# Kernel optimization log

Measured on AMD Instinct MI355X. Metric: run time of the kernel, lower is better.

## Reference

```python
import jax, jax.numpy as jnp
import numpy as np

NUM_TOKENS = 32
PAD_TOKEN = 1
DEL_COST = 1.0
INF = 1e9
EPS = 1e-7


def setup_inputs() -> dict:
    key = jax.random.key(0)
    k1, k2 = jax.random.split(key)
    y_true = jax.random.randint(k1, (32, 512), 0, NUM_TOKENS)
    y_pred = jax.random.uniform(k2, (32, 1024, NUM_TOKENS), dtype=jnp.float32)
    return {"y_true": y_true, "y_pred": y_pred}


def _left_shift(seq, pad_token):
    # remove internal pad tokens, shift real tokens left (stable)
    L = seq.shape[1]
    ixs = jnp.arange(L)
    keys = jnp.where(seq != pad_token, ixs[None, :], L + ixs[None, :])
    order = jnp.sort(keys, axis=1) % L
    return jnp.take_along_axis(seq, order, axis=1)


def _alignment(subs, ins, seq_lens):
    # subs: [b, m, n] substitution costs; ins: [b, n] insertion costs
    b, m, n = subs.shape
    dt = subs.dtype

    # wavefrontify subs -> [m+n-1, m, b]: out[k, i, :] = subs[:, i, k-i] (0 if oob)
    ks = jnp.arange(m + n - 1)[:, None]
    ii = jnp.arange(m)[None, :]
    jj = ks - ii
    subs_t = jnp.transpose(subs, (1, 2, 0))  # [m, n, b]
    subs_wf = jnp.where((jj >= 0) & (jj < n)[..., None] if False else ((jj >= 0) & (jj < n))[..., None],
                        subs_t[ii, jnp.clip(jj, 0, n - 1)], jnp.zeros((), dt))

    # wavefrontify ins -> [m+n, m+1, b]: out[k, i, :] = ins[:, k-i] (0 if oob)
    ks2 = jnp.arange(m + n)[:, None]
    ii2 = jnp.arange(m + 1)[None, :]
    jj2 = ks2 - ii2
    ins_t = jnp.transpose(ins, (1, 0))  # [n, b]
    ins_wf = jnp.where(((jj2 >= 0) & (jj2 < n))[..., None],
                       ins_t[jnp.clip(jj2, 0, n - 1)], jnp.zeros((), dt))

    i_range = jnp.arange(m + 1)
    batch_idx = jnp.arange(b)
    k_end = seq_lens + n  # antidiagonal where each sequence's answer lives

    # k=0 wavefront: D[0][0]=0 ; k=1 wavefront: D[0][1]=ins[0], D[1][0]=del
    v_p2 = jnp.concatenate([jnp.zeros((1, b), dt), jnp.full((m - 1, b), INF, dt)], 0)
    v_p1 = jnp.concatenate([ins_wf[0][:1], jnp.full((1, b), DEL_COST, dt),
                            jnp.full((m - 1, b), INF, dt)], 0)
    v_opt = jnp.full((b,), INF, dt)

    def step(carry, xs):
        v_p2, v_p1, v_opt = carry
        k, sub_k, ins_k = xs
        o_m = v_p2 + sub_k            # match:  D[i][j] + subs -> row i+1
        o_i = v_p1 + ins_k            # insert: D[i][j-1] + ins[j-1]
        v_p2n = v_p1[:-1]
        o_d = v_p2n + DEL_COST        # delete: D[i-1][j] + del
        rest = jnp.minimum(jnp.minimum(o_m, o_i[1:]), o_d)
        v_p1n = jnp.concatenate([o_i[:1], rest], 0)
        mask = ((k - i_range) >= 0) & ((k - i_range) <= n)
        v_p1n = jnp.where(mask[:, None], v_p1n, jnp.full((), INF, dt))
        v_opt = jnp.where(k_end == k, v_p1n[seq_lens, batch_idx], v_opt)
        return (v_p2n, v_p1n, v_opt), None

    ks_seq = jnp.arange(2, m + n + 1)
    (_, _, v_opt), _ = jax.lax.scan(step, (v_p2, v_p1, v_opt),
                                    (ks_seq, subs_wf, ins_wf[1:]))
    return v_opt


def reference(y_true, y_pred):
    y_true_ls = _left_shift(y_true, PAD_TOKEN)
    seq_lens = jnp.sum((y_true_ls != PAD_TOKEN).astype(jnp.int32), axis=-1)
    y_oh = jax.nn.one_hot(y_true_ls, NUM_TOKENS, dtype=y_pred.dtype)
    y_p = y_pred / jnp.sum(y_pred, axis=-1, keepdims=True)
    logp = jnp.log(jnp.clip(y_p, EPS, 1.0 - EPS))  # [b, n, t]
    subs = -jnp.einsum('bmt,bnt->bmn', y_oh, logp)  # sparse xent cost matrix
    ins = -jnp.log(jnp.clip(y_p[..., PAD_TOKEN], EPS, 1.0 - EPS))  # [b, n]
    loss = _alignment(subs, ins, seq_lens)
    return loss.sum()  # reduction='sum'
```

## Files before the change

### kernel.cpp

```cpp
#include <hip/hip_runtime.h>

#define NTOK 32
#define PADT 1
#define MLEN 512
#define NLEN 1024
#define EPS_F 1e-7f
#define CCH 256
#define NC 4
#define NWAVE 4
#define BSTRIDE 416

#define OFF_BND   0
#define OFF_P0    (OFF_BND + 4*2*BSTRIDE)
#define OFF_TOK   (OFF_P0 + 1184)
#define OFF_WTMP  (OFF_TOK + 512)
#define OFF_NL    (OFF_WTMP + 16)
#define LDS_FLOATS (OFF_NL + NTOK*NLEN + 160)

template <bool MASKED>
__device__ __forceinline__ void do_iter2(
    const float2*& q0, const float2*& q1, const float2*& qi, const float2*& qb,
    float2 (&C0)[8], float2 (&C1)[8], float2 (&CI)[8], float2 (&CB)[8],
    float2 (&N0)[8], float2 (&N1)[8], float2 (&NI)[8], float2 (&NB)[8],
    float& s0, float& s1, float& pA, float& dgA,
    int& sb, const int lane, float2* __restrict__ bw2)
{
#pragma unroll
  for (int k = 0; k < 8; ++k) {
    N0[k] = q0[8 + k]; N1[k] = q1[8 + k];
    NI[k] = qi[8 + k]; NB[k] = qb[8 + k];
  }
#pragma unroll
  for (int k = 0; k < 8; ++k) {
    float upA = __int_as_float(__builtin_amdgcn_update_dpp(
        __float_as_int(CB[k].x), __float_as_int(pA), 0x138, 0xF, 0xF, false));
    float upB = __int_as_float(__builtin_amdgcn_update_dpp(
        __float_as_int(CB[k].y), __float_as_int(s1), 0x138, 0xF, 0xF, false));
    float mA0 = fminf(fminf(dgA + C0[k].x, upA + 1.0f), s0 + CI[k].x);
    float mB0 = fminf(fminf(upA + C0[k].y, upB + 1.0f), mA0 + CI[k].y);
    float mA1 = fminf(fminf(s0  + C1[k].x, mA0 + 1.0f), s1 + CI[k].x);
    float mB1 = fminf(fminf(mA0 + C1[k].y, mB0 + 1.0f), mA1 + CI[k].y);
    if (lane == 63) {
      int sl = sb + k - 63;
      if (MASKED) sl = sl < 0 ? 0 : sl;
      bw2[sl] = make_float2(mA1, mB1);
    }
    if (MASKED) {
      int rsk = sb + k - lane;
      bool act = ((unsigned)rsk) < 128u;
      dgA = (rsk < 128) ? upB : dgA;
      s0 = act ? mB0 : s0;
      pA = act ? mA1 : pA;
      s1 = act ? mB1 : s1;
    } else {
      dgA = upB; s0 = mB0; pA = mA1; s1 = mB1;
    }
  }
  q0 += 8; q1 += 8; qi += 8; qb += 8; sb += 8;
}

__global__ __launch_bounds__(256, 1) void align_loss_kernel(
    const int* __restrict__ y_true, const float* __restrict__ y_pred,
    float* __restrict__ partial)
{
  extern __shared__ float smem[];
  float* bnd   = smem + OFF_BND;
  float* P0arr = smem + OFF_P0;
  int*   tok   = (int*)(smem + OFF_TOK);
  float* wtmp  = smem + OFF_WTMP;
  int*   wti   = (int*)wtmp;
  float* nl    = smem + OFF_NL;

  const int b = blockIdx.x;
  const int t = threadIdx.x;
  const int lane = t & 63;
  const int wv = t >> 6;

  tok[t] = 0; tok[t + 256] = 0;
  __syncthreads();
  int total = 0;
  for (int h = 0; h < 2; ++h) {
    int yt = y_true[b * MLEN + h * 256 + t];
    bool f = (yt != PADT);
    unsigned long long m = __ballot(f);
    int wp = __popcll(m & ((1ull << lane) - 1ull));
    if (lane == 0) wti[8 + wv] = __popcll(m);
    __syncthreads();
    int offs = total, ht = 0;
#pragma unroll
    for (int w2 = 0; w2 < NWAVE; ++w2) { int cnt = wti[8 + w2]; if (w2 < wv) offs += cnt; ht += cnt; }
    if (f) tok[offs + wp] = yt;
    total += ht;
    __syncthreads();
  }
  const int L = total;

  for (int r = t; r < NLEN; r += 256) {
    const float4* rp = (const float4*)(y_pred + ((size_t)b * NLEN + r) * NTOK);
    float4 q[8]; float s = 0.f;
#pragma unroll
    for (int u = 0; u < 8; ++u) { q[u] = rp[u]; s += q[u].x + q[u].y + q[u].z + q[u].w; }
    float inv = 1.0f / s;
#pragma unroll
    for (int u = 0; u < 8; ++u) {
      float pv[4] = {q[u].x, q[u].y, q[u].z, q[u].w};
#pragma unroll
      for (int c2 = 0; c2 < 4; ++c2) {
        float p = pv[c2] * inv;
        p = fminf(fmaxf(p, EPS_F), 1.0f - EPS_F);
        nl[(u * 4 + c2) * NLEN + r] = -__logf(p);
      }
    }
  }
  __syncthreads();

  {
    float4 iv = *(const float4*)(nl + PADT * NLEN + 4 * t);
    float p1 = iv.x, p2 = iv.x + iv.y, p3 = p2 + iv.z, s4 = p3 + iv.w;
    float x = s4;
#pragma unroll
    for (int d = 1; d < 64; d <<= 1) {
      float y = __shfl_up(x, d);
      if (lane >= d) x += y;
    }
    if (lane == 63) wtmp[wv] = x;
    __syncthreads();
    float pre = x - s4;
#pragma unroll
    for (int w2 = 0; w2 < NWAVE; ++w2) if (w2 < wv) pre += wtmp[w2];
    *(float4*)(P0arr + 4 * t) = make_float4(pre + p1, pre + p2, pre + p3, pre + s4);
  }

  const int r0 = 2 * t + 1;
  const int tk0 = tok[2 * t];
  const int tk1 = tok[2 * t + 1];
  const float* sub0 = nl + tk0 * NLEN;
  const float* sub1 = nl + tk1 * NLEN;
  const float* insp = nl + PADT * NLEN;
  float s0  = (float)r0;
  float s1  = (float)(r0 + 1);
  float dgA = (float)(r0 - 1);
  float pA  = (float)(r0 + 1);

  for (int p = 0; p < NC + NWAVE - 1; ++p) {
    __syncthreads();
    const int c = p - wv;
    if (c < 0 || c >= NC) continue;
    const int base = c * CCH;
    const float2* q0 = (const float2*)(sub0 + base) - lane;
    const float2* q1 = (const float2*)(sub1 + base) - lane;
    const float2* qi = (const float2*)(insp + base) - lane;
    const float2* qb = (wv == 0) ? (const float2*)(P0arr + base)
                                 : (const float2*)(bnd + ((wv - 1) * 2 + (p & 1)) * BSTRIDE);
    float2* bw2 = (float2*)(bnd + (wv * 2 + ((p + 1) & 1)) * BSTRIDE);

    float2 A0[8], A1[8], AI[8], AB[8], B0[8], B1[8], BI[8], BB[8];
#pragma unroll
    for (int k = 0; k < 8; ++k) { A0[k] = q0[k]; A1[k] = q1[k]; AI[k] = qi[k]; AB[k] = qb[k]; }
    int sb = 0;
    for (int it2 = 0; it2 < 4; ++it2) {
      do_iter2<true>(q0, q1, qi, qb, A0, A1, AI, AB, B0, B1, BI, BB, s0, s1, pA, dgA, sb, lane, bw2);
      do_iter2<true>(q0, q1, qi, qb, B0, B1, BI, BB, A0, A1, AI, AB, s0, s1, pA, dgA, sb, lane, bw2);
    }
    for (int it2 = 0; it2 < 4; ++it2) {
      do_iter2<false>(q0, q1, qi, qb, A0, A1, AI, AB, B0, B1, BI, BB, s0, s1, pA, dgA, sb, lane, bw2);
      do_iter2<false>(q0, q1, qi, qb, B0, B1, BI, BB, A0, A1, AI, AB, s0, s1, pA, dgA, sb, lane, bw2);
    }
    for (int it2 = 0; it2 < 4; ++it2) {
      do_iter2<true>(q0, q1, qi, qb, A0, A1, AI, AB, B0, B1, BI, BB, s0, s1, pA, dgA, sb, lane, bw2);
      do_iter2<true>(q0, q1, qi, qb, B0, B1, BI, BB, A0, A1, AI, AB, s0, s1, pA, dgA, sb, lane, bw2);
    }
  }

  if (r0 == L) partial[b] = s0;
  if (r0 + 1 == L) partial[b] = s1;
  if (L == 0 && t == 0) partial[b] = P0arr[NLEN - 1];
}

__global__ void reduce_kernel(const float* __restrict__ partial, float* __restrict__ out) {
  if (threadIdx.x == 0) {
    float s = 0.f;
    for (int b2 = 0; b2 < 32; ++b2) s += partial[b2];
    out[0] = s;
  }
}

extern "C" void kernel_launch(void* const* d_in, const int* in_sizes, int n_in,
                              void* d_out, int out_size, void* d_ws, size_t ws_size,
                              hipStream_t stream) {
  const int*   y_true = (const int*)d_in[0];
  const float* y_pred = (const float*)d_in[1];
  float* out = (float*)d_out;
  float* partial = (float*)d_ws;

  const size_t lds_bytes = (size_t)LDS_FLOATS * sizeof(float);
  hipFuncSetAttribute((const void*)align_loss_kernel,
                      hipFuncAttributeMaxDynamicSharedMemorySize, (int)lds_bytes);

  hipLaunchKernelGGL(align_loss_kernel, dim3(32), dim3(256), lds_bytes, stream,
                     y_true, y_pred, partial);
  hipLaunchKernelGGL(reduce_kernel, dim3(1), dim3(64), 0, stream, partial, out);
}
```

Measured before the change: 101.8 us.

## Transpose DP parallelization: lanes own prediction columns, sweep token rows

The wavefront DP is reorganized so that each lane owns four consecutive prediction positions (columns) and iterates over token rows in chunks of 128. Previously each lane owned two token rows and swept the prediction axis. Substitution costs are now fetched as float4 from the per-token log-prob table indexed by the row token, and the insertion cost becomes a per-lane constant. Boundary values pass between waves through LDS as float4 column-edge writes, and the answer is captured when the row index equals the sequence length. The aim is more work per lane per DPP shift and fewer LDS reads, at the price of token-indexed gathers and a new boundary protocol.

```diff
diff --git a/kernel.cpp b/kernel.cpp
--- a/kernel.cpp
+++ b/kernel.cpp
@@ -5,58 +5,79 @@
 #define MLEN 512
 #define NLEN 1024
 #define EPS_F 1e-7f
-#define CCH 256
-#define NC 4
+
+#define RCH 128
+#define NC  4
 #define NWAVE 4
-#define BSTRIDE 416
-
-#define OFF_BND   0
-#define OFF_P0    (OFF_BND + 4*2*BSTRIDE)
-#define OFF_TOK   (OFF_P0 + 1184)
-#define OFF_WTMP  (OFF_TOK + 512)
-#define OFF_NL    (OFF_WTMP + 16)
-#define LDS_FLOATS (OFF_NL + NTOK*NLEN + 160)
+#define NPHASE (NC + NWAVE - 1)
+
+#define OFF_P0   0
+#define OFF_BND  1024
+#define OFF_BNDZ (OFF_BND + 6*256)
+#define OFF_TOK  (OFF_BNDZ + 256)
+#define OFF_WT   (OFF_TOK + 736)
+#define OFF_NL   (OFF_WT + 16)
+#define LDS_FLOATS (OFF_NL + NTOK*NLEN)
+
+__device__ __forceinline__ float min3f(float a, float b, float c) {
+  return fminf(fminf(a, b), c);
+}
+__device__ __forceinline__ float dpp_shr1(float old_v, float src) {
+  return __int_as_float(__builtin_amdgcn_update_dpp(
+      __float_as_int(old_v), __float_as_int(src), 0x138, 0xF, 0xF, false));
+}
 
 template <bool MASKED>
-__device__ __forceinline__ void do_iter2(
-    const float2*& q0, const float2*& q1, const float2*& qi, const float2*& qb,
-    float2 (&C0)[8], float2 (&C1)[8], float2 (&CI)[8], float2 (&CB)[8],
-    float2 (&N0)[8], float2 (&N1)[8], float2 (&NI)[8], float2 (&NB)[8],
-    float& s0, float& s1, float& pA, float& dgA,
-    int& sb, const int lane, float2* __restrict__ bw2)
+__device__ __forceinline__ void do_iter(
+    int s0, int lane, int wv,
+    const int* __restrict__ tokl, const float* __restrict__ nlJ,
+    const float* __restrict__ bndR, float* __restrict__ bndW,
+    int (&TKc)[8], float4 (&SBc)[8], int (&TKn)[8], float4 (&SBn)[8],
+    float4 ri,
+    float& vp0, float& vp1, float& vp2, float& vp3,
+    float& dgL, float& m3p,
+    float& wq0, float& wq1, float& wq2, float& wq3,
+    float& ans, int qh)
 {
 #pragma unroll
+  for (int k = 0; k < 8; ++k) TKn[k] = tokl[s0 + 16 + k];
+#pragma unroll
+  for (int k = 0; k < 8; ++k)
+    SBn[k] = *(const float4*)(nlJ + ((size_t)((unsigned)TKc[k]) << 10));
+  float4 ja = *(const float4*)(bndR + s0);
+  float4 jb = *(const float4*)(bndR + s0 + 4);
+  float inj[8] = {ja.x, ja.y, ja.z, ja.w, jb.x, jb.y, jb.z, jb.w};
+  const int q0 = s0 - lane;
+#pragma unroll
   for (int k = 0; k < 8; ++k) {
-    N0[k] = q0[8 + k]; N1[k] = q1[8 + k];
-    NI[k] = qi[8 + k]; NB[k] = qb[8 + k];
-  }
-#pragma unroll
-  for (int k = 0; k < 8; ++k) {
-    float upA = __int_as_float(__builtin_amdgcn_update_dpp(
-        __float_as_int(CB[k].x), __float_as_int(pA), 0x138, 0xF, 0xF, false));
-    float upB = __int_as_float(__builtin_amdgcn_update_dpp(
-        __float_as_int(CB[k].y), __float_as_int(s1), 0x138, 0xF, 0xF, false));
-    float mA0 = fminf(fminf(dgA + C0[k].x, upA + 1.0f), s0 + CI[k].x);
-    float mB0 = fminf(fminf(upA + C0[k].y, upB + 1.0f), mA0 + CI[k].y);
-    float mA1 = fminf(fminf(s0  + C1[k].x, mA0 + 1.0f), s1 + CI[k].x);
-    float mB1 = fminf(fminf(mA0 + C1[k].y, mB0 + 1.0f), mA1 + CI[k].y);
-    if (lane == 63) {
-      int sl = sb + k - 63;
-      if (MASKED) sl = sl < 0 ? 0 : sl;
-      bw2[sl] = make_float2(mA1, mB1);
-    }
+    const int q = q0 + k;
+    float Lnow = dpp_shr1(inj[k], m3p);
+    float m0 = min3f(dgL + SBc[k].x, vp0 + 1.0f, Lnow + ri.x);
+    float m1 = min3f(vp0 + SBc[k].y, vp1 + 1.0f, m0 + ri.y);
+    float m2 = min3f(vp1 + SBc[k].z, vp2 + 1.0f, m1 + ri.z);
+    float m3 = min3f(vp2 + SBc[k].w, vp3 + 1.0f, m2 + ri.w);
     if (MASKED) {
-      int rsk = sb + k - lane;
-      bool act = ((unsigned)rsk) < 128u;
-      dgA = (rsk < 128) ? upB : dgA;
-      s0 = act ? mB0 : s0;
-      pA = act ? mA1 : pA;
-      s1 = act ? mB1 : s1;
+      bool act = ((unsigned)q) < 128u;
+      bool lt  = (q < 128);
+      dgL = lt ? Lnow : dgL;
+      vp0 = act ? m0 : vp0;  vp1 = act ? m1 : vp1;
+      vp2 = act ? m2 : vp2;  vp3 = act ? m3 : vp3;
+      m3p = act ? m3 : m3p;
+      if (act && q == qh) ans = m3;
     } else {
-      dgA = upB; s0 = mB0; pA = mA1; s1 = mB1;
-    }
-  }
-  q0 += 8; q1 += 8; qi += 8; qb += 8; sb += 8;
+      dgL = Lnow; vp0 = m0; vp1 = m1; vp2 = m2; vp3 = m3; m3p = m3;
+      if (q == qh) ans = m3;
+    }
+    switch ((k + 1) & 3) {
+      case 0: wq0 = m3; break; case 1: wq1 = m3; break;
+      case 2: wq2 = m3; break; case 3: wq3 = m3; break;
+    }
+    if (k == 2 || k == 6) {
+      int q63 = s0 + k - 63;
+      if (wv < 3 && lane == 63 && q63 >= 3 && q63 < 128)
+        *(float4*)(bndW + (q63 - 3)) = make_float4(wq0, wq1, wq2, wq3);
+    }
+  }
 }
 
 __global__ __launch_bounds__(256, 1) void align_loss_kernel(
@@ -64,10 +85,12 @@
     float* __restrict__ partial)
 {
   extern __shared__ float smem[];
+  float* P0    = smem + OFF_P0;
   float* bnd   = smem + OFF_BND;
-  float* P0arr = smem + OFF_P0;
-  int*   tok   = (int*)(smem + OFF_TOK);
-  float* wtmp  = smem + OFF_WTMP;
+  float* bndZ  = smem + OFF_BNDZ;
+  int*   tokbuf= (int*)(smem + OFF_TOK);
+  int*   tokg  = tokbuf + 64;
+  float* wtmp  = smem + OFF_WT;
   int*   wti   = (int*)wtmp;
   float* nl    = smem + OFF_NL;
 
@@ -76,8 +99,9 @@
   const int lane = t & 63;
   const int wv = t >> 6;
 
-  tok[t] = 0; tok[t + 256] = 0;
+  for (int idx = t; idx < 736; idx += 256) tokbuf[idx] = 0;
   __syncthreads();
+
   int total = 0;
   for (int h = 0; h < 2; ++h) {
     int yt = y_true[b * MLEN + h * 256 + t];
@@ -89,7 +113,7 @@
     int offs = total, ht = 0;
 #pragma unroll
     for (int w2 = 0; w2 < NWAVE; ++w2) { int cnt = wti[8 + w2]; if (w2 < wv) offs += cnt; ht += cnt; }
-    if (f) tok[offs + wp] = yt;
+    if (f) tokg[offs + wp] = yt;
     total += ht;
     __syncthreads();
   }
@@ -128,53 +152,66 @@
     float pre = x - s4;
 #pragma unroll
     for (int w2 = 0; w2 < NWAVE; ++w2) if (w2 < wv) pre += wtmp[w2];
-    *(float4*)(P0arr + 4 * t) = make_float4(pre + p1, pre + p2, pre + p3, pre + s4);
-  }
-
-  const int r0 = 2 * t + 1;
-  const int tk0 = tok[2 * t];
-  const int tk1 = tok[2 * t + 1];
-  const float* sub0 = nl + tk0 * NLEN;
-  const float* sub1 = nl + tk1 * NLEN;
-  const float* insp = nl + PADT * NLEN;
-  float s0  = (float)r0;
-  float s1  = (float)(r0 + 1);
-  float dgA = (float)(r0 - 1);
-  float pA  = (float)(r0 + 1);
-
-  for (int p = 0; p < NC + NWAVE - 1; ++p) {
+    *(float4*)(P0 + 4 * t) = make_float4(pre + p1, pre + p2, pre + p3, pre + s4);
+  }
+  __syncthreads();
+
+  const int J = 256 * wv + 4 * lane;
+  const float* nlJ = nl + J;
+  float4 ri = *(const float4*)(nl + PADT * NLEN + J);
+  float4 vpi = *(const float4*)(P0 + J);
+  float vp0 = vpi.x, vp1 = vpi.y, vp2 = vpi.z, vp3 = vpi.w;
+  float m3p = vp3;
+  float dgL = 0.0f;
+  if (J > 0) dgL = P0[J - 1];
+  float wq0 = 0, wq1 = 0, wq2 = 0, wq3 = 0, ans = 0.0f;
+
+  for (int p = 0; p < NPHASE; ++p) {
     __syncthreads();
     const int c = p - wv;
     if (c < 0 || c >= NC) continue;
-    const int base = c * CCH;
-    const float2* q0 = (const float2*)(sub0 + base) - lane;
-    const float2* q1 = (const float2*)(sub1 + base) - lane;
-    const float2* qi = (const float2*)(insp + base) - lane;
-    const float2* qb = (wv == 0) ? (const float2*)(P0arr + base)
-                                 : (const float2*)(bnd + ((wv - 1) * 2 + (p & 1)) * BSTRIDE);
-    float2* bw2 = (float2*)(bnd + (wv * 2 + ((p + 1) & 1)) * BSTRIDE);
-
-    float2 A0[8], A1[8], AI[8], AB[8], B0[8], B1[8], BI[8], BB[8];
-#pragma unroll
-    for (int k = 0; k < 8; ++k) { A0[k] = q0[k]; A1[k] = q1[k]; AI[k] = qi[k]; AB[k] = qb[k]; }
-    int sb = 0;
-    for (int it2 = 0; it2 < 4; ++it2) {
-      do_iter2<true>(q0, q1, qi, qb, A0, A1, AI, AB, B0, B1, BI, BB, s0, s1, pA, dgA, sb, lane, bw2);
-      do_iter2<true>(q0, q1, qi, qb, B0, B1, BI, BB, A0, A1, AI, AB, s0, s1, pA, dgA, sb, lane, bw2);
-    }
-    for (int it2 = 0; it2 < 4; ++it2) {
-      do_iter2<false>(q0, q1, qi, qb, A0, A1, AI, AB, B0, B1, BI, BB, s0, s1, pA, dgA, sb, lane, bw2);
-      do_iter2<false>(q0, q1, qi, qb, B0, B1, BI, BB, A0, A1, AI, AB, s0, s1, pA, dgA, sb, lane, bw2);
-    }
-    for (int it2 = 0; it2 < 4; ++it2) {
-      do_iter2<true>(q0, q1, qi, qb, A0, A1, AI, AB, B0, B1, BI, BB, s0, s1, pA, dgA, sb, lane, bw2);
-      do_iter2<true>(q0, q1, qi, qb, B0, B1, BI, BB, A0, A1, AI, AB, s0, s1, pA, dgA, sb, lane, bw2);
-    }
-  }
-
-  if (r0 == L) partial[b] = s0;
-  if (r0 + 1 == L) partial[b] = s1;
-  if (L == 0 && t == 0) partial[b] = P0arr[NLEN - 1];
+    const int* tokl = tokg + c * RCH - lane;
+    const float* bndR = (wv == 0) ? bndZ : (bnd + ((wv - 1) * 2 + (c & 1)) * 256);
+    float* bndW = bnd + (wv * 2 + (c & 1)) * 256;
+    const int qh = L - 1 - c * RCH;
+    if (wv == 0) {
+      float base = (float)(c * RCH + 1);
+      bndZ[lane]       = base + (float)lane;
+      bndZ[lane + 64]  = base + (float)(lane + 64);
+      bndZ[lane + 128] = base + (float)(lane + 128);
+      bndZ[lane + 192] = base + (float)(lane + 192);
+    }
+    int tk0[8], TKa[8], TKb[8]; float4 SBa[8], SBb[8];
+#pragma unroll
+    for (int k = 0; k < 8; ++k) tk0[k] = tokl[k];
+#pragma unroll
+    for (int k = 0; k < 8; ++k) SBa[k] = *(const float4*)(nlJ + ((size_t)((unsigned)tk0[k]) << 10));
+#pragma unroll
+    for (int k = 0; k < 8; ++k) TKa[k] = tokl[8 + k];
+
+    int s0 = 0;
+    for (int pr = 0; pr < 4; ++pr) {
+      do_iter<true>(s0, lane, wv, tokl, nlJ, bndR, bndW, TKa, SBa, TKb, SBb, ri,
+                    vp0, vp1, vp2, vp3, dgL, m3p, wq0, wq1, wq2, wq3, ans, qh); s0 += 8;
+      do_iter<true>(s0, lane, wv, tokl, nlJ, bndR, bndW, TKb, SBb, TKa, SBa, ri,
+                    vp0, vp1, vp2, vp3, dgL, m3p, wq0, wq1, wq2, wq3, ans, qh); s0 += 8;
+    }
+    for (int pr = 0; pr < 4; ++pr) {
+      do_iter<false>(s0, lane, wv, tokl, nlJ, bndR, bndW, TKa, SBa, TKb, SBb, ri,
+                     vp0, vp1, vp2, vp3, dgL, m3p, wq0, wq1, wq2, wq3, ans, qh); s0 += 8;
+      do_iter<false>(s0, lane, wv, tokl, nlJ, bndR, bndW, TKb, SBb, TKa, SBa, ri,
+                     vp0, vp1, vp2, vp3, dgL, m3p, wq0, wq1, wq2, wq3, ans, qh); s0 += 8;
+    }
+    for (int pr = 0; pr < 4; ++pr) {
+      do_iter<true>(s0, lane, wv, tokl, nlJ, bndR, bndW, TKa, SBa, TKb, SBb, ri,
+                    vp0, vp1, vp2, vp3, dgL, m3p, wq0, wq1, wq2, wq3, ans, qh); s0 += 8;
+      do_iter<true>(s0, lane, wv, tokl, nlJ, bndR, bndW, TKb, SBb, TKa, SBa, ri,
+                    vp0, vp1, vp2, vp3, dgL, m3p, wq0, wq1, wq2, wq3, ans, qh); s0 += 8;
+    }
+  }
+
+  if (t == 255) partial[b] = ans;
+  if (L == 0 && t == 0) partial[b] = P0[NLEN - 1];
 }
 
 __global__ void reduce_kernel(const float* __restrict__ partial, float* __restrict__ out) {
```

Result: faster. 97.52 us (-4.2%).
